# Performance work log

Measured on AMD Instinct MI355X. Metric: run time of the kernel, lower is better.

The kernel has to match this reference:

```python
import jax, jax.numpy as jnp
import numpy as np

DEPTH = 4096
BATCH = 16384


def fwht(x):
    """Normalized fast Walsh-Hadamard transform along the last axis.
    x: [B, n], n a power of two. Returns H @ x rows, scaled by 1/sqrt(n).
    """
    B, n = x.shape
    h = 1
    while h < n:
        # combine elements i and i+h within blocks of size 2h (butterfly)
        x = x.reshape(B, n // (2 * h), 2, h)
        a = x[..., 0, :]
        b = x[..., 1, :]
        x = jnp.concatenate([a + b, a - b], axis=-1).reshape(B, n)
        h *= 2
    return x * (1.0 / jnp.sqrt(jnp.asarray(n, x.dtype)))


def setup_inputs() -> dict:
    key = jax.random.key(0)
    kx, kp = jax.random.split(key)
    x = jax.random.normal(kx, (BATCH, DEPTH), dtype=jnp.float32)
    # learned diagonal vectors S, G, B initialized to ones as in the module
    diag_s = jnp.ones((DEPTH,), dtype=jnp.float32)
    diag_g = jnp.ones((DEPTH,), dtype=jnp.float32)
    diag_b = jnp.ones((DEPTH,), dtype=jnp.float32)
    # random permutation: torch.mm(y, P) with P a row-permuted identity is a
    # column gather y[:, idx] for idx = argsort(pi); idx itself is a uniform
    # random permutation, so we draw it directly.
    perm_idx = jax.random.permutation(kp, jnp.arange(DEPTH, dtype=jnp.int32))
    return {"x": x, "diag_s": diag_s, "diag_g": diag_g, "diag_b": diag_b,
            "perm_idx": perm_idx}


def reference(x, diag_s, diag_g, diag_b, perm_idx):
    # forward: S * H * G * P * H * B  (dropout in eval mode -> identity)
    y = x * diag_b                 # mul_b: diagonal scale
    y = fwht(y)                    # first Walsh-Hadamard transform
    y = jnp.take(y, perm_idx, axis=1)  # mul_p: column permutation
    y = y * diag_g                 # mul_g
    y = fwht(y)                    # second Walsh-Hadamard transform
    y = y * diag_s                 # mul_s
    return y
```

## Files before the change

### kernel.cpp

```cpp
#include <hip/hip_runtime.h>

#define FF_N 4096
#define S64  0.015625f

typedef float  v2f __attribute__((ext_vector_type(2)));
typedef __fp16 pkhalf2 __attribute__((ext_vector_type(2)));

__device__ __forceinline__ v2f pk_add(v2f a, v2f b) {
    v2f d; asm("v_pk_add_f32 %0, %1, %2" : "=v"(d) : "v"(a), "v"(b)); return d;
}
__device__ __forceinline__ v2f pk_sub(v2f a, v2f b) {
    v2f d; asm("v_pk_add_f32 %0, %1, %2 neg_lo:[0,1] neg_hi:[0,1]"
               : "=v"(d) : "v"(a), "v"(b)); return d;
}
__device__ __forceinline__ void h16p(v2f v[16]) {
#pragma unroll
    for (int b = 1; b < 16; b <<= 1) {
#pragma unroll
        for (int r = 0; r < 16; ++r) {
            if ((r & b) == 0) {
                const v2f u = v[r], w = v[r | b];
                v[r]     = pk_add(u, w);
                v[r | b] = pk_sub(u, w);
            }
        }
    }
}

__device__ __forceinline__ unsigned pkpack(v2f a) {
    union { pkhalf2 h; unsigned u; } cv;
    cv.h = __builtin_amdgcn_cvt_pkrtz(a[0], a[1]);
    return cv.u;
}
__device__ __forceinline__ v2f pkunpack(unsigned u) {
    union { unsigned u; pkhalf2 h; } cv; cv.u = u;
    return (v2f){(float)cv.h[0], (float)cv.h[1]};
}


__global__ void ff_setup(const float* __restrict__ diag_s,
                         const float* __restrict__ diag_g,
                         const int*   __restrict__ perm,
                         int*   __restrict__ gaddr,
                         float* __restrict__ gg,
                         float* __restrict__ ss) {
    const int k   = blockIdx.x * 256 + threadIdx.x;
    const int pe  = perm[k];
    const int d2p = pe >> 8, d1p = (pe >> 4) & 15, d0p = pe & 15;
    gaddr[k] = (d1p << 8) | ((d0p >> 3) << 7) | ((d2p >> 2) << 5)
             | (((d0p & 7) ^ (d2p >> 2)) << 2) | (d2p & 3);
    gg[k] = diag_g[k] * S64;
    ss[k] = diag_s[k] * S64;
}

__global__ __launch_bounds__(256, 6) void fastfood_h16_kernel(
    const float* __restrict__ x,
    const float* __restrict__ diag_b,
    const int*   __restrict__ gaddr,
    const float* __restrict__ gg,
    const float* __restrict__ ss,
    float* __restrict__ out)
{
    __shared__ __align__(16) unsigned L[FF_N];
    const int t = threadIdx.x;
    const int T = t >> 4, c = t & 15;
    const size_t rowA = (size_t)blockIdx.x * 2;
    const float* __restrict__ xA   = x   + rowA * FF_N;
    const float* __restrict__ xB   = xA  + FF_N;
    float* __restrict__       outA = out + rowA * FF_N;
    float* __restrict__       outB = outA + FF_N;

    int WB[4];
#pragma unroll
    for (int q = 0; q < 4; ++q)
        WB[q] = (T << 8) | ((c >> 3) << 7) | (q << 5) | ((((c & 7) ^ q)) << 2);
    const int AR0 = (T << 8) | ((c >> 2) << 5) | (c & 3);
    const int PR0 = ((c >> 3) << 7) | ((T >> 2) << 5)
                  | ((((c & 7) ^ (T >> 2))) << 2) | (T & 3);

    v2f v[16];

#define JWRITE()                                                               \
    {                                                                          \
        _Pragma("unroll")                                                      \
        for (int q = 0; q < 4; ++q) {                                          \
            uint4 w;                                                           \
            w.x = pkpack(v[4 * q + 0]); w.y = pkpack(v[4 * q + 1]);            \
            w.z = pkpack(v[4 * q + 2]); w.w = pkpack(v[4 * q + 3]);            \
            *(uint4*)&L[WB[q]] = w;                                            \
        }                                                                      \
    }

    {
        const float4* __restrict__ xa4 = (const float4*)(xA + 16 * t);
        const float4* __restrict__ xb4 = (const float4*)(xB + 16 * t);
        const float4* __restrict__ b4  = (const float4*)(diag_b + 16 * t);
#pragma unroll
        for (int q = 0; q < 4; ++q) {
            const float4 bv = b4[q];
            const float4 av = xa4[q];
            const float4 wv = xb4[q];
            v[4 * q + 0] = (v2f){av.x * bv.x, wv.x * bv.x};
            v[4 * q + 1] = (v2f){av.y * bv.y, wv.y * bv.y};
            v[4 * q + 2] = (v2f){av.z * bv.z, wv.z * bv.z};
            v[4 * q + 3] = (v2f){av.w * bv.w, wv.w * bv.w};
        }
        h16p(v);
        JWRITE();
    }
    __syncthreads();

#pragma unroll
    for (int j = 0; j < 16; ++j)
        v[j] = pkunpack(L[AR0 | ((j >> 3) << 7) | ((((j & 7) ^ (c >> 2))) << 2)]);
    h16p(v);
    __syncthreads();
    JWRITE();
    __syncthreads();

#pragma unroll
    for (int j = 0; j < 16; ++j)
        v[j] = pkunpack(L[PR0 | (j << 8)]);
    h16p(v);
    __syncthreads();
    JWRITE();
    __syncthreads();

    {
        const int4*   __restrict__ ga4 = (const int4*)(gaddr + 16 * t);
        const float4* __restrict__ gg4 = (const float4*)(gg + 16 * t);
#pragma unroll
        for (int q = 0; q < 4; ++q) {
            const int4   pa = ga4[q];
            const float4 gv = gg4[q];
            const v2f a0 = pkunpack(L[pa.x]), a1 = pkunpack(L[pa.y]);
            const v2f a2 = pkunpack(L[pa.z]), a3 = pkunpack(L[pa.w]);
            v[4 * q + 0] = (v2f){a0[0] * gv.x, a0[1] * gv.x};
            v[4 * q + 1] = (v2f){a1[0] * gv.y, a1[1] * gv.y};
            v[4 * q + 2] = (v2f){a2[0] * gv.z, a2[1] * gv.z};
            v[4 * q + 3] = (v2f){a3[0] * gv.w, a3[1] * gv.w};
        }
        h16p(v);
    }
    __syncthreads();
    JWRITE();
    __syncthreads();

#pragma unroll
    for (int j = 0; j < 16; ++j)
        v[j] = pkunpack(L[AR0 | ((j >> 3) << 7) | ((((j & 7) ^ (c >> 2))) << 2)]);
    h16p(v);
    __syncthreads();
    JWRITE();
    __syncthreads();

#pragma unroll
    for (int j = 0; j < 16; ++j)
        v[j] = pkunpack(L[PR0 | (j << 8)]);
    h16p(v);
#pragma unroll
    for (int j = 0; j < 16; ++j) {
        const int e = 256 * j + t;
        const float s = ss[e];
        __builtin_nontemporal_store(v[j][0] * s, &outA[e]);
        __builtin_nontemporal_store(v[j][1] * s, &outB[e]);
    }
#undef JWRITE
}

extern "C" void kernel_launch(void* const* d_in, const int* in_sizes, int n_in,
                              void* d_out, int out_size, void* d_ws, size_t ws_size,
                              hipStream_t stream) {
    const float* x      = (const float*)d_in[0];
    const float* diag_s = (const float*)d_in[1];
    const float* diag_g = (const float*)d_in[2];
    const float* diag_b = (const float*)d_in[3];
    const int*   perm   = (const int*)d_in[4];
    float* out = (float*)d_out;

    int*   gaddr = (int*)d_ws;
    float* gg    = (float*)d_ws + FF_N;
    float* ss    = (float*)d_ws + 2 * FF_N;

    ff_setup<<<FF_N / 256, 256, 0, stream>>>(diag_s, diag_g, perm, gaddr, gg, ss);

    const int batch = in_sizes[0] / FF_N;
    fastfood_h16_kernel<<<batch / 2, 256, 0, stream>>>(x, diag_b, gaddr, gg, ss, out);
}
```

Baseline: 93.10 us.

## Process four rows per block, prefetching second row pair during first pair's compute

Each block now handles four rows instead of two. The x values for the second pair of rows are loaded into registers before the first pair's transform pipeline runs, so the global load latency overlaps with the shared-memory butterfly work. The grid is half the size. The extra 32 live floats per thread raise register pressure under the same launch bounds (6 blocks of 256), which may cause spills or lower occupancy.

```diff
diff --git a/kernel.cpp b/kernel.cpp
--- a/kernel.cpp
+++ b/kernel.cpp
@@ -53,7 +53,86 @@
     ss[k] = diag_s[k] * S64;
 }
 
-__global__ __launch_bounds__(256, 6) void fastfood_h16_kernel(
+__device__ __forceinline__ void jwrite(const v2f v[16], unsigned* __restrict__ L,
+                                       const int WB[4]) {
+#pragma unroll
+    for (int q = 0; q < 4; ++q) {
+        uint4 w;
+        w.x = pkpack(v[4 * q + 0]); w.y = pkpack(v[4 * q + 1]);
+        w.z = pkpack(v[4 * q + 2]); w.w = pkpack(v[4 * q + 3]);
+        *(uint4*)&L[WB[q]] = w;
+    }
+}
+
+__device__ __forceinline__ void ff_tail(
+    v2f v[16], unsigned* __restrict__ L, const int WB[4],
+    const int AR0, const int PR0,
+    const int*   __restrict__ gaddr,
+    const float* __restrict__ gg,
+    const float* __restrict__ ss,
+    const int t, const int c,
+    float* __restrict__ outA, float* __restrict__ outB)
+{
+    h16p(v);
+    jwrite(v, L, WB);
+    __syncthreads();
+
+#pragma unroll
+    for (int j = 0; j < 16; ++j)
+        v[j] = pkunpack(L[AR0 | ((j >> 3) << 7) | (((j & 7) ^ (c >> 2)) << 2)]);
+    h16p(v);
+    __syncthreads();
+    jwrite(v, L, WB);
+    __syncthreads();
+
+#pragma unroll
+    for (int j = 0; j < 16; ++j) v[j] = pkunpack(L[PR0 | (j << 8)]);
+    h16p(v);
+    __syncthreads();
+    jwrite(v, L, WB);
+    __syncthreads();
+
+    {
+        const int4*   __restrict__ ga4 = (const int4*)(gaddr + 16 * t);
+        const float4* __restrict__ gg4 = (const float4*)(gg + 16 * t);
+#pragma unroll
+        for (int q = 0; q < 4; ++q) {
+            const int4   pa = ga4[q];
+            const float4 gv = gg4[q];
+            const v2f a0 = pkunpack(L[pa.x]), a1 = pkunpack(L[pa.y]);
+            const v2f a2 = pkunpack(L[pa.z]), a3 = pkunpack(L[pa.w]);
+            v[4 * q + 0] = (v2f){a0[0] * gv.x, a0[1] * gv.x};
+            v[4 * q + 1] = (v2f){a1[0] * gv.y, a1[1] * gv.y};
+            v[4 * q + 2] = (v2f){a2[0] * gv.z, a2[1] * gv.z};
+            v[4 * q + 3] = (v2f){a3[0] * gv.w, a3[1] * gv.w};
+        }
+        h16p(v);
+    }
+    __syncthreads();
+    jwrite(v, L, WB);
+    __syncthreads();
+
+#pragma unroll
+    for (int j = 0; j < 16; ++j)
+        v[j] = pkunpack(L[AR0 | ((j >> 3) << 7) | (((j & 7) ^ (c >> 2)) << 2)]);
+    h16p(v);
+    __syncthreads();
+    jwrite(v, L, WB);
+    __syncthreads();
+
+#pragma unroll
+    for (int j = 0; j < 16; ++j) v[j] = pkunpack(L[PR0 | (j << 8)]);
+    h16p(v);
+#pragma unroll
+    for (int j = 0; j < 16; ++j) {
+        const int e = 256 * j + t;
+        const float s = ss[e];
+        __builtin_nontemporal_store(v[j][0] * s, &outA[e]);
+        __builtin_nontemporal_store(v[j][1] * s, &outB[e]);
+    }
+}
+
+__global__ __launch_bounds__(256, 6) void fastfood_pp_kernel(
     const float* __restrict__ x,
     const float* __restrict__ diag_b,
     const int*   __restrict__ gaddr,
@@ -64,32 +143,25 @@
     __shared__ __align__(16) unsigned L[FF_N];
     const int t = threadIdx.x;
     const int T = t >> 4, c = t & 15;
-    const size_t rowA = (size_t)blockIdx.x * 2;
-    const float* __restrict__ xA   = x   + rowA * FF_N;
-    const float* __restrict__ xB   = xA  + FF_N;
-    float* __restrict__       outA = out + rowA * FF_N;
-    float* __restrict__       outB = outA + FF_N;
+    const size_t row0 = (size_t)blockIdx.x * 4;
+    const float* __restrict__ xA = x + row0 * FF_N;
+    const float* __restrict__ xB = xA + FF_N;
+    const float* __restrict__ xC = xB + FF_N;
+    const float* __restrict__ xD = xC + FF_N;
+    float* __restrict__ oA = out + row0 * FF_N;
+    float* __restrict__ oB = oA + FF_N;
+    float* __restrict__ oC = oB + FF_N;
+    float* __restrict__ oD = oC + FF_N;
 
     int WB[4];
 #pragma unroll
     for (int q = 0; q < 4; ++q)
-        WB[q] = (T << 8) | ((c >> 3) << 7) | (q << 5) | ((((c & 7) ^ q)) << 2);
+        WB[q] = (T << 8) | ((c >> 3) << 7) | (q << 5) | (((c & 7) ^ q) << 2);
     const int AR0 = (T << 8) | ((c >> 2) << 5) | (c & 3);
     const int PR0 = ((c >> 3) << 7) | ((T >> 2) << 5)
-                  | ((((c & 7) ^ (T >> 2))) << 2) | (T & 3);
+                  | (((c & 7) ^ (T >> 2)) << 2) | (T & 3);
 
     v2f v[16];
-
-#define JWRITE()                                                               \
-    {                                                                          \
-        _Pragma("unroll")                                                      \
-        for (int q = 0; q < 4; ++q) {                                          \
-            uint4 w;                                                           \
-            w.x = pkpack(v[4 * q + 0]); w.y = pkpack(v[4 * q + 1]);            \
-            w.z = pkpack(v[4 * q + 2]); w.w = pkpack(v[4 * q + 3]);            \
-            *(uint4*)&L[WB[q]] = w;                                            \
-        }                                                                      \
-    }
 
     {
         const float4* __restrict__ xa4 = (const float4*)(xA + 16 * t);
@@ -105,67 +177,33 @@
             v[4 * q + 2] = (v2f){av.z * bv.z, wv.z * bv.z};
             v[4 * q + 3] = (v2f){av.w * bv.w, wv.w * bv.w};
         }
-        h16p(v);
-        JWRITE();
-    }
-    __syncthreads();
-
-#pragma unroll
-    for (int j = 0; j < 16; ++j)
-        v[j] = pkunpack(L[AR0 | ((j >> 3) << 7) | ((((j & 7) ^ (c >> 2))) << 2)]);
-    h16p(v);
-    __syncthreads();
-    JWRITE();
-    __syncthreads();
-
-#pragma unroll
-    for (int j = 0; j < 16; ++j)
-        v[j] = pkunpack(L[PR0 | (j << 8)]);
-    h16p(v);
-    __syncthreads();
-    JWRITE();
-    __syncthreads();
-
-    {
-        const int4*   __restrict__ ga4 = (const int4*)(gaddr + 16 * t);
-        const float4* __restrict__ gg4 = (const float4*)(gg + 16 * t);
+    }
+
+    float4 rc[4], rd[4];
+    {
+        const float4* __restrict__ xc4 = (const float4*)(xC + 16 * t);
+        const float4* __restrict__ xd4 = (const float4*)(xD + 16 * t);
+#pragma unroll
+        for (int q = 0; q < 4; ++q) { rc[q] = xc4[q]; rd[q] = xd4[q]; }
+    }
+
+    ff_tail(v, L, WB, AR0, PR0, gaddr, gg, ss, t, c, oA, oB);
+
+    __syncthreads();
+
+    {
+        const float4* __restrict__ b4 = (const float4*)(diag_b + 16 * t);
 #pragma unroll
         for (int q = 0; q < 4; ++q) {
-            const int4   pa = ga4[q];
-            const float4 gv = gg4[q];
-            const v2f a0 = pkunpack(L[pa.x]), a1 = pkunpack(L[pa.y]);
-            const v2f a2 = pkunpack(L[pa.z]), a3 = pkunpack(L[pa.w]);
-            v[4 * q + 0] = (v2f){a0[0] * gv.x, a0[1] * gv.x};
-            v[4 * q + 1] = (v2f){a1[0] * gv.y, a1[1] * gv.y};
-            v[4 * q + 2] = (v2f){a2[0] * gv.z, a2[1] * gv.z};
-            v[4 * q + 3] = (v2f){a3[0] * gv.w, a3[1] * gv.w};
-        }
-        h16p(v);
-    }
-    __syncthreads();
-    JWRITE();
-    __syncthreads();
-
-#pragma unroll
-    for (int j = 0; j < 16; ++j)
-        v[j] = pkunpack(L[AR0 | ((j >> 3) << 7) | ((((j & 7) ^ (c >> 2))) << 2)]);
-    h16p(v);
-    __syncthreads();
-    JWRITE();
-    __syncthreads();
-
-#pragma unroll
-    for (int j = 0; j < 16; ++j)
-        v[j] = pkunpack(L[PR0 | (j << 8)]);
-    h16p(v);
-#pragma unroll
-    for (int j = 0; j < 16; ++j) {
-        const int e = 256 * j + t;
-        const float s = ss[e];
-        __builtin_nontemporal_store(v[j][0] * s, &outA[e]);
-        __builtin_nontemporal_store(v[j][1] * s, &outB[e]);
-    }
-#undef JWRITE
+            const float4 bv = b4[q];
+            v[4 * q + 0] = (v2f){rc[q].x * bv.x, rd[q].x * bv.x};
+            v[4 * q + 1] = (v2f){rc[q].y * bv.y, rd[q].y * bv.y};
+            v[4 * q + 2] = (v2f){rc[q].z * bv.z, rd[q].z * bv.z};
+            v[4 * q + 3] = (v2f){rc[q].w * bv.w, rd[q].w * bv.w};
+        }
+    }
+
+    ff_tail(v, L, WB, AR0, PR0, gaddr, gg, ss, t, c, oC, oD);
 }
 
 extern "C" void kernel_launch(void* const* d_in, const int* in_sizes, int n_in,
@@ -185,5 +223,5 @@
     ff_setup<<<FF_N / 256, 256, 0, stream>>>(diag_s, diag_g, perm, gaddr, gg, ss);
 
     const int batch = in_sizes[0] / FF_N;
-    fastfood_h16_kernel<<<batch / 2, 256, 0, stream>>>(x, diag_b, gaddr, gg, ss, out);
-}
+    fastfood_pp_kernel<<<batch / 4, 256, 0, stream>>>(x, diag_b, gaddr, gg, ss, out);
+}
```

Result: slower. 151.3 us (+62.6%).
